# Kernel optimization log

Hardware: AMD Instinct MI355X
Metric: run time of the kernel (lower is better)

## Reference

```python
import jax, jax.numpy as jnp
import numpy as np

N_NODES = 50000
N_EDGES = 600000
H_DIM = 128


def setup_inputs() -> dict:
    key = jax.random.key(0)
    ks = jax.random.split(key, 16)
    s = 0.05  # weight scale
    inp = {
        'h': jax.random.normal(ks[0], (N_NODES, H_DIM), jnp.float32),
        'coord': jax.random.normal(ks[1], (N_NODES, 3), jnp.float32),
        'edge_index': jax.random.randint(ks[2], (2, N_EDGES), 0, N_NODES, jnp.int32),
        # edge_mlp: (2*input_nf + 1) -> hidden -> hidden
        'w_e1': jax.random.normal(ks[3], (2 * H_DIM + 1, H_DIM), jnp.float32) * s,
        'b_e1': jnp.zeros((H_DIM,), jnp.float32),
        'w_e2': jax.random.normal(ks[4], (H_DIM, H_DIM), jnp.float32) * s,
        'b_e2': jnp.zeros((H_DIM,), jnp.float32),
        # node_mlp: (hidden + input_nf) -> hidden -> output_nf
        'w_n1': jax.random.normal(ks[5], (2 * H_DIM, H_DIM), jnp.float32) * s,
        'b_n1': jnp.zeros((H_DIM,), jnp.float32),
        'w_n2': jax.random.normal(ks[6], (H_DIM, H_DIM), jnp.float32) * s,
        'b_n2': jnp.zeros((H_DIM,), jnp.float32),
        # coord_mlp: hidden -> hidden -> 1 (last layer xavier gain 0.001, no bias)
        'w_c1': jax.random.normal(ks[7], (H_DIM, H_DIM), jnp.float32) * s,
        'b_c1': jnp.zeros((H_DIM,), jnp.float32),
        'w_c2': jax.random.normal(ks[8], (H_DIM, 1), jnp.float32) * 0.001,
    }
    return inp


def reference(h, coord, edge_index, w_e1, b_e1, w_e2, b_e2,
              w_n1, b_n1, w_n2, b_n2, w_c1, b_c1, w_c2):
    silu = jax.nn.silu
    n = h.shape[0]
    row, col = edge_index[0], edge_index[1]

    # coord2radial (normalize=False)
    coord_diff = coord[row] - coord[col]                 # [E, 3]
    radial = jnp.sum(coord_diff ** 2, axis=1, keepdims=True)  # [E, 1]

    # edge model (no attention, no edge_attr)
    edge_in = jnp.concatenate([h[row], h[col], radial], axis=1)  # [E, 257]
    edge_feat = silu(silu(edge_in @ w_e1 + b_e1) @ w_e2 + b_e2)  # [E, H]

    # coord model: coords_agg='mean', tanh=False
    w = silu(edge_feat @ w_c1 + b_c1) @ w_c2             # [E, 1]
    trans = coord_diff * w                               # [E, 3]
    t_sum = jax.ops.segment_sum(trans, row, num_segments=n)
    cnt = jax.ops.segment_sum(jnp.ones((row.shape[0], 1), trans.dtype), row,
                              num_segments=n)
    coord_new = coord + t_sum / jnp.maximum(cnt, 1.0)

    # node model (residual=True, no graphnorm, no node attention)
    agg = jax.ops.segment_sum(edge_feat, row, num_segments=n)   # [N, H]
    node_in = jnp.concatenate([h, agg], axis=1)                 # [N, 2H]
    h_new = h + (silu(node_in @ w_n1 + b_n1) @ w_n2 + b_n2)

    return (h_new, coord_new, edge_feat)
```

## Files before the change

kernel.cpp:

```cpp
#include <hip/hip_runtime.h>

#define NN 50000
#define NE 600000

typedef __attribute__((ext_vector_type(8))) short short8;
typedef __attribute__((ext_vector_type(4))) float f32x4;

#define SWZ(row) ((((row) & 7) << 4) ^ (((row) & 8) << 2))

__device__ __forceinline__ float silu_f(float x) { return x / (1.0f + __expf(-x)); }

__device__ __forceinline__ unsigned short f2bf(float f) {
    unsigned u = __builtin_bit_cast(unsigned, f);
    unsigned r = u + 0x7FFFu + ((u >> 16) & 1u);
    return (unsigned short)(r >> 16);
}

__device__ __forceinline__ void lds_barrier() {
    asm volatile("s_waitcnt lgkmcnt(0)" ::: "memory");
    __builtin_amdgcn_s_barrier();
    asm volatile("" ::: "memory");
}

__global__ __launch_bounds__(512) void k_prep(const float* __restrict__ h,
                                              unsigned short* __restrict__ hb)
{
    const int nchunks = NN * 128 / 8;
    for (int i = blockIdx.x * blockDim.x + threadIdx.x; i < nchunks;
         i += gridDim.x * blockDim.x) {
        const float4* p = (const float4*)(h + (size_t)i * 8);
        float4 x = p[0], y = p[1];
        short8 v;
        v[0] = f2bf(x.x); v[1] = f2bf(x.y); v[2] = f2bf(x.z); v[3] = f2bf(x.w);
        v[4] = f2bf(y.x); v[5] = f2bf(y.y); v[6] = f2bf(y.z); v[7] = f2bf(y.w);
        *(short8*)(hb + (size_t)i * 8) = v;
    }
}

__global__ __launch_bounds__(512, 4) void k_edge(
    const unsigned short* __restrict__ hb, const float* __restrict__ coord,
    const int* __restrict__ ei,
    const float* __restrict__ w_e1, const float* __restrict__ b_e1,
    const float* __restrict__ w_e2, const float* __restrict__ b_e2,
    const float* __restrict__ w_c1, const float* __restrict__ b_c1,
    const float* __restrict__ w_c2,
    float* __restrict__ ef, float* __restrict__ agg,
    float* __restrict__ tsum, float* __restrict__ cnt)
{
    __shared__ unsigned short A1s[64 * 256];
    __shared__ unsigned short A2s[64 * 128];
    __shared__ float rad[64];
    __shared__ float dxyz[64][3];
    __shared__ int   rows_s[64];
    __shared__ float wqp[8][64];

    const int tid  = threadIdx.x;
    const int wv   = tid >> 6, lane = tid & 63;
    const int l4   = lane >> 4, li = lane & 15;
    const int n    = wv * 16 + li;

    short8 bw1[8], bw2[4], bwc[4];
    #pragma unroll
    for (int ks = 0; ks < 8; ++ks) {
        short8 t;
        #pragma unroll
        for (int j = 0; j < 8; ++j) t[j] = f2bf(w_e1[(ks * 32 + l4 * 8 + j) * 128 + n]);
        bw1[ks] = t;
    }
    #pragma unroll
    for (int ks = 0; ks < 4; ++ks) {
        short8 t, u;
        #pragma unroll
        for (int j = 0; j < 8; ++j) {
            t[j] = f2bf(w_e2[(ks * 32 + l4 * 8 + j) * 128 + n]);
            u[j] = f2bf(w_c1[(ks * 32 + l4 * 8 + j) * 128 + n]);
        }
        bw2[ks] = t; bwc[ks] = u;
    }
    const float wradv = w_e1[256 * 128 + n];
    const float b1v = b_e1[n], b2v = b_e2[n], bc1v = b_c1[n], wc2v = w_c2[n];

    const f32x4 z4 = {0.f, 0.f, 0.f, 0.f};

    for (int t = blockIdx.x; t < NE / 64; t += gridDim.x) {
        const int ebase = t * 64;
        if (tid < 64) {
            int e = ebase + tid;
            int r = ei[e], c = ei[NE + e];
            rows_s[tid] = r;
            float dx = coord[r * 3 + 0] - coord[c * 3 + 0];
            float dy = coord[r * 3 + 1] - coord[c * 3 + 1];
            float dz = coord[r * 3 + 2] - coord[c * 3 + 2];
            dxyz[tid][0] = dx; dxyz[tid][1] = dy; dxyz[tid][2] = dz;
            rad[tid] = dx * dx + dy * dy + dz * dz;
        }
        {
            int le = tid >> 3;
            int e = ebase + le;
            int r = ei[e], c = ei[NE + e];
            const unsigned short* hr = hb + (size_t)r * 128;
            const unsigned short* hc = hb + (size_t)c * 128;
            #pragma unroll
            for (int i = 0; i < 4; ++i) {
                int chunk = i * 8 + (tid & 7);
                short8 v = (chunk < 16) ? *(const short8*)(hr + chunk * 8)
                                        : *(const short8*)(hc + (chunk - 16) * 8);
                int off = le * 512 + ((chunk * 16) ^ SWZ(le));
                *(short8*)((char*)A1s + off) = v;
            }
        }
        lds_barrier();

        f32x4 acc[4];
        acc[0] = z4; acc[1] = z4; acc[2] = z4; acc[3] = z4;
        for (int ks = 0; ks < 8; ++ks) {
            const int kb = ks * 64 + l4 * 16;
            #pragma unroll
            for (int mf = 0; mf < 4; ++mf) {
                int row = mf * 16 + li;
                short8 a = *(const short8*)((const char*)A1s + row * 512 + (kb ^ SWZ(row)));
                acc[mf] = __builtin_amdgcn_mfma_f32_16x16x32_bf16(a, bw1[ks], acc[mf], 0, 0, 0);
            }
        }
        #pragma unroll
        for (int mf = 0; mf < 4; ++mf)
            #pragma unroll
            for (int r = 0; r < 4; ++r) {
                int row = mf * 16 + l4 * 4 + r;
                float v = silu_f(acc[mf][r] + rad[row] * wradv + b1v);
                int off = row * 256 + ((n * 2) ^ SWZ(row));
                *(unsigned short*)((char*)A2s + off) = f2bf(v);
            }
        lds_barrier();

        acc[0] = z4; acc[1] = z4; acc[2] = z4; acc[3] = z4;
        for (int ks = 0; ks < 4; ++ks) {
            const int kb = ks * 64 + l4 * 16;
            #pragma unroll
            for (int mf = 0; mf < 4; ++mf) {
                int row = mf * 16 + li;
                short8 a = *(const short8*)((const char*)A2s + row * 256 + (kb ^ SWZ(row)));
                acc[mf] = __builtin_amdgcn_mfma_f32_16x16x32_bf16(a, bw2[ks], acc[mf], 0, 0, 0);
            }
        }
        #pragma unroll
        for (int mf = 0; mf < 4; ++mf)
            #pragma unroll
            for (int r = 0; r < 4; ++r) {
                int row = mf * 16 + l4 * 4 + r;
                int e = ebase + row;
                float v = silu_f(acc[mf][r] + b2v);
                int off = row * 256 + ((n * 2) ^ SWZ(row));
                *(unsigned short*)((char*)A1s + off) = f2bf(v);
                __builtin_nontemporal_store(v, &ef[(size_t)e * 128 + n]);
                atomicAdd(&agg[(size_t)rows_s[row] * 128 + n], v);
            }
        lds_barrier();

        acc[0] = z4; acc[1] = z4; acc[2] = z4; acc[3] = z4;
        for (int ks = 0; ks < 4; ++ks) {
            const int kb = ks * 64 + l4 * 16;
            #pragma unroll
            for (int mf = 0; mf < 4; ++mf) {
                int row = mf * 16 + li;
                short8 a = *(const short8*)((const char*)A1s + row * 256 + (kb ^ SWZ(row)));
                acc[mf] = __builtin_amdgcn_mfma_f32_16x16x32_bf16(a, bwc[ks], acc[mf], 0, 0, 0);
            }
        }
        #pragma unroll
        for (int mf = 0; mf < 4; ++mf)
            #pragma unroll
            for (int r = 0; r < 4; ++r) {
                float p = silu_f(acc[mf][r] + bc1v) * wc2v;
                p += __shfl_xor(p, 1); p += __shfl_xor(p, 2);
                p += __shfl_xor(p, 4); p += __shfl_xor(p, 8);
                if (li == 0) wqp[wv][mf * 16 + l4 * 4 + r] = p;
            }
        lds_barrier();

        if (tid < 64) {
            float wq = 0.f;
            #pragma unroll
            for (int w = 0; w < 8; ++w) wq += wqp[w][tid];
            int rr = rows_s[tid];
            atomicAdd(&tsum[rr * 3 + 0], dxyz[tid][0] * wq);
            atomicAdd(&tsum[rr * 3 + 1], dxyz[tid][1] * wq);
            atomicAdd(&tsum[rr * 3 + 2], dxyz[tid][2] * wq);
            atomicAdd(&cnt[rr], 1.0f);
        }
    }
}

__global__ __launch_bounds__(512, 4) void k_node(
    const unsigned short* __restrict__ hb, const float* __restrict__ h,
    const float* __restrict__ agg,
    const float* __restrict__ w_n1, const float* __restrict__ b_n1,
    const float* __restrict__ w_n2, const float* __restrict__ b_n2,
    const float* __restrict__ coord, const float* __restrict__ tsum,
    const float* __restrict__ cnt,
    float* __restrict__ h_new, float* __restrict__ coord_new)
{
    __shared__ unsigned short As[64 * 256];
    __shared__ unsigned short Us[64 * 128];

    const int tid  = threadIdx.x;
    const int wv   = tid >> 6, lane = tid & 63;
    const int l4   = lane >> 4, li = lane & 15;
    const int n    = wv * 16 + li;

    short8 bw1[8], bw2[4];
    #pragma unroll
    for (int ks = 0; ks < 8; ++ks) {
        short8 t;
        #pragma unroll
        for (int j = 0; j < 8; ++j) t[j] = f2bf(w_n1[(ks * 32 + l4 * 8 + j) * 128 + n]);
        bw1[ks] = t;
    }
    #pragma unroll
    for (int ks = 0; ks < 4; ++ks) {
        short8 t;
        #pragma unroll
        for (int j = 0; j < 8; ++j) t[j] = f2bf(w_n2[(ks * 32 + l4 * 8 + j) * 128 + n]);
        bw2[ks] = t;
    }
    const float b1v = b_n1[n], b2v = b_n2[n];

    const f32x4 z4 = {0.f, 0.f, 0.f, 0.f};
    const int ntiles = (NN + 63) / 64;

    for (int t = blockIdx.x; t < ntiles; t += gridDim.x) {
        const int nbase = t * 64;
        {
            int ln = tid >> 3;
            int node = nbase + ln;
            #pragma unroll
            for (int i = 0; i < 4; ++i) {
                int chunk = i * 8 + (tid & 7);
                short8 v;
                if (node < NN) {
                    if (chunk < 16) {
                        v = *(const short8*)(hb + (size_t)node * 128 + chunk * 8);
                    } else {
                        const float4* p = (const float4*)(agg + (size_t)node * 128 + (chunk - 16) * 8);
                        float4 x = p[0], y = p[1];
                        v[0] = f2bf(x.x); v[1] = f2bf(x.y); v[2] = f2bf(x.z); v[3] = f2bf(x.w);
                        v[4] = f2bf(y.x); v[5] = f2bf(y.y); v[6] = f2bf(y.z); v[7] = f2bf(y.w);
                    }
                } else v = (short8)0;
                int off = ln * 512 + ((chunk * 16) ^ SWZ(ln));
                *(short8*)((char*)As + off) = v;
            }
        }
        lds_barrier();

        f32x4 acc[4];
        acc[0] = z4; acc[1] = z4; acc[2] = z4; acc[3] = z4;
        for (int ks = 0; ks < 8; ++ks) {
            const int kb = ks * 64 + l4 * 16;
            #pragma unroll
            for (int mf = 0; mf < 4; ++mf) {
                int row = mf * 16 + li;
                short8 a = *(const short8*)((const char*)As + row * 512 + (kb ^ SWZ(row)));
                acc[mf] = __builtin_amdgcn_mfma_f32_16x16x32_bf16(a, bw1[ks], acc[mf], 0, 0, 0);
            }
        }
        #pragma unroll
        for (int mf = 0; mf < 4; ++mf)
            #pragma unroll
            for (int r = 0; r < 4; ++r) {
                int row = mf * 16 + l4 * 4 + r;
                float v = silu_f(acc[mf][r] + b1v);
                int off = row * 256 + ((n * 2) ^ SWZ(row));
                *(unsigned short*)((char*)Us + off) = f2bf(v);
            }
        lds_barrier();

        acc[0] = z4; acc[1] = z4; acc[2] = z4; acc[3] = z4;
        for (int ks = 0; ks < 4; ++ks) {
            const int kb = ks * 64 + l4 * 16;
            #pragma unroll
            for (int mf = 0; mf < 4; ++mf) {
                int row = mf * 16 + li;
                short8 a = *(const short8*)((const char*)Us + row * 256 + (kb ^ SWZ(row)));
                acc[mf] = __builtin_amdgcn_mfma_f32_16x16x32_bf16(a, bw2[ks], acc[mf], 0, 0, 0);
            }
        }
        #pragma unroll
        for (int mf = 0; mf < 4; ++mf)
            #pragma unroll
            for (int r = 0; r < 4; ++r) {
                int row = mf * 16 + l4 * 4 + r;
                int node = nbase + row;
                if (node < NN) {
                    float v = acc[mf][r] + b2v + h[(size_t)node * 128 + n];
                    __builtin_nontemporal_store(v, &h_new[(size_t)node * 128 + n]);
                }
            }
        if (tid < 64) {
            int node = nbase + tid;
            if (node < NN) {
                float m = fmaxf(cnt[node], 1.0f);
                coord_new[node * 3 + 0] = coord[node * 3 + 0] + tsum[node * 3 + 0] / m;
                coord_new[node * 3 + 1] = coord[node * 3 + 1] + tsum[node * 3 + 1] / m;
                coord_new[node * 3 + 2] = coord[node * 3 + 2] + tsum[node * 3 + 2] / m;
            }
        }
    }
}

extern "C" void kernel_launch(void* const* d_in, const int* in_sizes, int n_in,
                              void* d_out, int out_size, void* d_ws, size_t ws_size,
                              hipStream_t stream)
{
    const float* h     = (const float*)d_in[0];
    const float* coord = (const float*)d_in[1];
    const int*   ei    = (const int*)d_in[2];
    const float* w_e1  = (const float*)d_in[3];
    const float* b_e1  = (const float*)d_in[4];
    const float* w_e2  = (const float*)d_in[5];
    const float* b_e2  = (const float*)d_in[6];
    const float* w_n1  = (const float*)d_in[7];
    const float* b_n1  = (const float*)d_in[8];
    const float* w_n2  = (const float*)d_in[9];
    const float* b_n2  = (const float*)d_in[10];
    const float* w_c1  = (const float*)d_in[11];
    const float* b_c1  = (const float*)d_in[12];
    const float* w_c2  = (const float*)d_in[13];

    float* h_new     = (float*)d_out;
    float* coord_new = h_new + (size_t)NN * 128;
    float* ef        = coord_new + (size_t)NN * 3;

    float*          agg  = (float*)d_ws;
    float*          tsum = agg + (size_t)NN * 128;
    float*          cnt  = tsum + (size_t)NN * 3;
    unsigned short* hb   = (unsigned short*)(cnt + NN);

    hipMemsetAsync(agg, 0, ((size_t)NN * 128 + (size_t)NN * 3 + NN) * sizeof(float), stream);

    k_prep<<<1024, 512, 0, stream>>>(h, hb);
    k_edge<<<512, 512, 0, stream>>>(hb, coord, ei, w_e1, b_e1, w_e2, b_e2,
                                    w_c1, b_c1, w_c2, ef, agg, tsum, cnt);
    k_node<<<512, 512, 0, stream>>>(hb, h, agg, w_n1, b_n1, w_n2, b_n2,
                                    coord, tsum, cnt, h_new, coord_new);
}
```

Baseline: 544.4 us.

## Replace atomic scatter-add with CSR-based gather aggregation per node

Builds a CSR edge list grouped by row (degree count, single-block scan, scatter) and drops the per-element float atomics into agg, tsum and cnt from the edge kernel. The edge kernel now writes edge features normally and stores per-edge coordinate translations. A new kernel then gathers those per node, one wave per node, to form agg and coord_new. This trades contended global atomics for extra passes: a re-read of the 307 MB edge feature tensor, several small launches and a serial single-block scan.

```diff
diff --git a/kernel.cpp b/kernel.cpp
--- a/kernel.cpp
+++ b/kernel.cpp
@@ -37,6 +37,56 @@
     }
 }
 
+__global__ __launch_bounds__(256) void k_deg(const int* __restrict__ ei,
+                                             int* __restrict__ deg)
+{
+    for (int e = blockIdx.x * 256 + threadIdx.x; e < NE; e += gridDim.x * 256)
+        atomicAdd(&deg[ei[e]], 1);
+}
+
+__global__ __launch_bounds__(1024) void k_scan(const int* __restrict__ deg,
+                                               int* __restrict__ rowptr,
+                                               int* __restrict__ cursor)
+{
+    __shared__ int sb[1024];
+    const int t = threadIdx.x;
+    const int CH = 49;
+    const int base = t * CH;
+    int s = 0;
+    for (int j = 0; j < CH; ++j) {
+        int idx = base + j;
+        if (idx < NN) s += deg[idx];
+    }
+    sb[t] = s;
+    __syncthreads();
+    for (int off = 1; off < 1024; off <<= 1) {
+        int v = (t >= off) ? sb[t - off] : 0;
+        __syncthreads();
+        sb[t] += v;
+        __syncthreads();
+    }
+    int run = sb[t] - s;
+    for (int j = 0; j < CH; ++j) {
+        int idx = base + j;
+        if (idx < NN) {
+            rowptr[idx] = run;
+            cursor[idx] = run;
+            run += deg[idx];
+        }
+    }
+    if (t == 1023) rowptr[NN] = sb[1023];
+}
+
+__global__ __launch_bounds__(256) void k_scatter(const int* __restrict__ ei,
+                                                 int* __restrict__ cursor,
+                                                 int* __restrict__ elist)
+{
+    for (int e = blockIdx.x * 256 + threadIdx.x; e < NE; e += gridDim.x * 256) {
+        int pos = atomicAdd(&cursor[ei[e]], 1);
+        elist[pos] = e;
+    }
+}
+
 __global__ __launch_bounds__(512, 4) void k_edge(
     const unsigned short* __restrict__ hb, const float* __restrict__ coord,
     const int* __restrict__ ei,
@@ -44,14 +94,12 @@
     const float* __restrict__ w_e2, const float* __restrict__ b_e2,
     const float* __restrict__ w_c1, const float* __restrict__ b_c1,
     const float* __restrict__ w_c2,
-    float* __restrict__ ef, float* __restrict__ agg,
-    float* __restrict__ tsum, float* __restrict__ cnt)
+    float* __restrict__ ef, float* __restrict__ trans)
 {
     __shared__ unsigned short A1s[64 * 256];
     __shared__ unsigned short A2s[64 * 128];
     __shared__ float rad[64];
     __shared__ float dxyz[64][3];
-    __shared__ int   rows_s[64];
     __shared__ float wqp[8][64];
 
     const int tid  = threadIdx.x;
@@ -87,7 +135,6 @@
         if (tid < 64) {
             int e = ebase + tid;
             int r = ei[e], c = ei[NE + e];
-            rows_s[tid] = r;
             float dx = coord[r * 3 + 0] - coord[c * 3 + 0];
             float dy = coord[r * 3 + 1] - coord[c * 3 + 1];
             float dz = coord[r * 3 + 2] - coord[c * 3 + 2];
@@ -152,8 +199,7 @@
                 float v = silu_f(acc[mf][r] + b2v);
                 int off = row * 256 + ((n * 2) ^ SWZ(row));
                 *(unsigned short*)((char*)A1s + off) = f2bf(v);
-                __builtin_nontemporal_store(v, &ef[(size_t)e * 128 + n]);
-                atomicAdd(&agg[(size_t)rows_s[row] * 128 + n], v);
+                ef[(size_t)e * 128 + n] = v;
             }
         lds_barrier();
 
@@ -182,11 +228,37 @@
             float wq = 0.f;
             #pragma unroll
             for (int w = 0; w < 8; ++w) wq += wqp[w][tid];
-            int rr = rows_s[tid];
-            atomicAdd(&tsum[rr * 3 + 0], dxyz[tid][0] * wq);
-            atomicAdd(&tsum[rr * 3 + 1], dxyz[tid][1] * wq);
-            atomicAdd(&tsum[rr * 3 + 2], dxyz[tid][2] * wq);
-            atomicAdd(&cnt[rr], 1.0f);
+            int e = ebase + tid;
+            trans[(size_t)e * 3 + 0] = dxyz[tid][0] * wq;
+            trans[(size_t)e * 3 + 1] = dxyz[tid][1] * wq;
+            trans[(size_t)e * 3 + 2] = dxyz[tid][2] * wq;
+        }
+    }
+}
+
+__global__ __launch_bounds__(512) void k_agg(
+    const float* __restrict__ ef, const float* __restrict__ trans,
+    const int* __restrict__ rowptr, const int* __restrict__ elist,
+    const float* __restrict__ coord,
+    float* __restrict__ agg, float* __restrict__ coord_new)
+{
+    const int wv = threadIdx.x >> 6, lane = threadIdx.x & 63;
+    const int nw = gridDim.x * 8;
+    for (int node = blockIdx.x * 8 + wv; node < NN; node += nw) {
+        const int s = rowptr[node], e2 = rowptr[node + 1];
+        float a0 = 0.f, a1 = 0.f;
+        for (int i = s; i < e2; ++i) {
+            int e = elist[i];
+            a0 += ef[(size_t)e * 128 + lane];
+            a1 += ef[(size_t)e * 128 + 64 + lane];
+        }
+        agg[(size_t)node * 128 + lane]      = a0;
+        agg[(size_t)node * 128 + 64 + lane] = a1;
+        if (lane < 3) {
+            float ts = 0.f;
+            for (int i = s; i < e2; ++i) ts += trans[(size_t)elist[i] * 3 + lane];
+            coord_new[node * 3 + lane] =
+                coord[node * 3 + lane] + ts / fmaxf((float)(e2 - s), 1.f);
         }
     }
 }
@@ -196,9 +268,7 @@
     const float* __restrict__ agg,
     const float* __restrict__ w_n1, const float* __restrict__ b_n1,
     const float* __restrict__ w_n2, const float* __restrict__ b_n2,
-    const float* __restrict__ coord, const float* __restrict__ tsum,
-    const float* __restrict__ cnt,
-    float* __restrict__ h_new, float* __restrict__ coord_new)
+    float* __restrict__ h_new)
 {
     __shared__ unsigned short As[64 * 256];
     __shared__ unsigned short Us[64 * 128];
@@ -296,15 +366,6 @@
                     __builtin_nontemporal_store(v, &h_new[(size_t)node * 128 + n]);
                 }
             }
-        if (tid < 64) {
-            int node = nbase + tid;
-            if (node < NN) {
-                float m = fmaxf(cnt[node], 1.0f);
-                coord_new[node * 3 + 0] = coord[node * 3 + 0] + tsum[node * 3 + 0] / m;
-                coord_new[node * 3 + 1] = coord[node * 3 + 1] + tsum[node * 3 + 1] / m;
-                coord_new[node * 3 + 2] = coord[node * 3 + 2] + tsum[node * 3 + 2] / m;
-            }
-        }
     }
 }
 
@@ -331,16 +392,23 @@
     float* coord_new = h_new + (size_t)NN * 128;
     float* ef        = coord_new + (size_t)NN * 3;
 
-    float*          agg  = (float*)d_ws;
-    float*          tsum = agg + (size_t)NN * 128;
-    float*          cnt  = tsum + (size_t)NN * 3;
-    unsigned short* hb   = (unsigned short*)(cnt + NN);
-
-    hipMemsetAsync(agg, 0, ((size_t)NN * 128 + (size_t)NN * 3 + NN) * sizeof(float), stream);
-
-    k_prep<<<1024, 512, 0, stream>>>(h, hb);
-    k_edge<<<512, 512, 0, stream>>>(hb, coord, ei, w_e1, b_e1, w_e2, b_e2,
-                                    w_c1, b_c1, w_c2, ef, agg, tsum, cnt);
-    k_node<<<512, 512, 0, stream>>>(hb, h, agg, w_n1, b_n1, w_n2, b_n2,
-                                    coord, tsum, cnt, h_new, coord_new);
-}
+    float*          agg    = (float*)d_ws;
+    unsigned short* hb     = (unsigned short*)(agg + (size_t)NN * 128);
+    float*          trans  = (float*)(hb + (size_t)NN * 128);
+    int*            deg    = (int*)(trans + (size_t)NE * 3);
+    int*            rowptr = deg + NN;
+    int*            cursor = rowptr + NN + 1;
+    int*            elist  = cursor + NN;
+
+    hipMemsetAsync(deg, 0, NN * sizeof(int), stream);
+
+    k_prep   <<<1024, 512, 0, stream>>>(h, hb);
+    k_deg    <<<1024, 256, 0, stream>>>(ei, deg);
+    k_scan   <<<1,   1024, 0, stream>>>(deg, rowptr, cursor);
+    k_scatter<<<1024, 256, 0, stream>>>(ei, cursor, elist);
+    k_edge   <<<512,  512, 0, stream>>>(hb, coord, ei, w_e1, b_e1, w_e2, b_e2,
+                                        w_c1, b_c1, w_c2, ef, trans);
+    k_agg    <<<2048, 512, 0, stream>>>(ef, trans, rowptr, elist, coord,
+                                        agg, coord_new);
+    k_node   <<<512,  512, 0, stream>>>(hb, h, agg, w_n1, b_n1, w_n2, b_n2, h_new);
+}
```

After: 832.8 us. 1.53x slower.
